# Performance work log

Measured on AMD Instinct MI355X. Metric: run time of the kernel, lower is better.

## Reference

```python
import jax, jax.numpy as jnp
import numpy as np

N = 100000      # nodes
E = 1200000     # edges (avg degree ~12)
D_IN = 64
D_OUT = 64


def setup_inputs() -> dict:
    key = jax.random.key(0)
    k1, k2, k3, k4 = jax.random.split(key, 4)
    x = jax.random.normal(k1, (N, D_IN), dtype=jnp.float32)
    # learned params (glorot-ish init)
    W = jax.random.normal(k2, (D_IN, D_OUT), dtype=jnp.float32) / np.sqrt(D_IN).astype(np.float32)
    b = jnp.zeros((D_OUT,), dtype=jnp.float32)
    src = jax.random.randint(k3, (E,), 0, N, dtype=jnp.int32)
    dst = jax.random.randint(k4, (E,), 0, N, dtype=jnp.int32)
    return {"x": x, "W": W, "b": b, "src": src, "dst": dst}


def reference(x, W, b, src, dst):
    # GCN layer: h = relu( D^-1/2 A D^-1/2 (x @ W) + b ), dropout=0 (eval)
    ones = jnp.ones(src.shape[0], dtype=x.dtype)
    deg_out = jax.ops.segment_sum(ones, src, num_segments=N)   # out-degree of source nodes
    deg_in = jax.ops.segment_sum(ones, dst, num_segments=N)    # in-degree of dest nodes
    norm_src = jax.lax.rsqrt(jnp.maximum(deg_out, 1.0))
    norm_dst = jax.lax.rsqrt(jnp.maximum(deg_in, 1.0))

    h = x @ W                                                  # [N, D_OUT] dense transform
    msg = h[src] * norm_src[src][:, None]                      # [E, D_OUT] gathered, pre-normalized messages
    agg = jax.ops.segment_sum(msg, dst, num_segments=N)        # [N, D_OUT] sparse aggregation
    out = agg * norm_dst[:, None] + b
    return jax.nn.relu(out)
```

## Files before the change

### kernel.cpp

```cpp
#include <hip/hip_runtime.h>
#include <hip/hip_bf16.h>

#define N_NODES 100000
#define N_EDGES 1200000
#define DCH 64

#define HB 96
#define CHUNK ((N_EDGES + HB - 1) / HB)
#define HALF_BINS 50000
#define HALF_WORDS 12500

#define BNODES 256
#define KBUK ((N_NODES + BNODES - 1) / BNODES)
#define CAPE 6144

#define GEMMB 384

#define OFF_DEG      0
#define OFF_CNTR     100000
#define OFF_BPART    512000
#define OFF_BLOCKOFF 665600
#define OFF_FLAG     819200
#define OFF_ESORT    819456
#define OFF_HS       10419712

__device__ __forceinline__ float load_f(const void* p, int i, int f32) {
    if (f32) return ((const float*)p)[i];
    return __bfloat162float(((const __hip_bfloat16*)p)[i]);
}

__device__ __forceinline__ unsigned short f2bf_bits(float f) {
    __hip_bfloat16 h = __float2bfloat16(f);
    return __builtin_bit_cast(unsigned short, h);
}

__global__ __launch_bounds__(1024)
void edges_kernel(const int* __restrict__ src,
                  const int* __restrict__ dst,
                  const void* __restrict__ x,
                  unsigned int* __restrict__ deg_packed,
                  int* __restrict__ bpart,
                  int* __restrict__ blockoff,
                  int* __restrict__ counter,
                  int* __restrict__ flag) {
    __shared__ unsigned int h[HALF_WORDS];
    __shared__ int cnt[KBUK];
    __shared__ int ss[512];
    __shared__ int amlast;
    int tid = threadIdx.x, b = blockIdx.x, half = blockIdx.y;
    for (int w = tid; w < HALF_WORDS; w += 1024) h[w] = 0;
    if (half == 0)
        for (int i = tid; i < KBUK; i += 1024) cnt[i] = 0;
    __syncthreads();
    int lo = half * HALF_BINS;
    int e0 = b * CHUNK;
    const int2* src2 = (const int2*)(src + e0);
    const int2* dst2 = (const int2*)(dst + e0);
    int npair = CHUNK >> 1;
    for (int p = tid; p < npair; p += 1024) {
        int2 sp = src2[p];
        int n0 = sp.x - lo, n1 = sp.y - lo;
        if ((unsigned)n0 < (unsigned)HALF_BINS)
            atomicAdd(&h[n0 >> 2], 1u << ((n0 & 3) * 8));
        if ((unsigned)n1 < (unsigned)HALF_BINS)
            atomicAdd(&h[n1 >> 2], 1u << ((n1 & 3) * 8));
        if (half == 0) {
            int2 dp = dst2[p];
            atomicAdd(&cnt[dp.x >> 8], 1);
            atomicAdd(&cnt[dp.y >> 8], 1);
        }
    }
    __syncthreads();
    unsigned int* dp = deg_packed + half * HALF_WORDS;
    for (int w = tid; w < HALF_WORDS; w += 1024) {
        unsigned int v = h[w];
        if (v) atomicAdd(&dp[w], v);
    }
    if (half == 0)
        for (int i = tid; i < KBUK; i += 1024) bpart[b * KBUK + i] = cnt[i];

    if (b == 0 && half == 0) {
        __syncthreads();
        if (tid == 0) cnt[0] = 0;
        __syncthreads();
        if (tid < 256) {
            const unsigned short* u = (const unsigned short*)x;
            int c = 0;
            for (int i = tid * 16; i < tid * 16 + 16; ++i) {
                unsigned short v = u[2 * i];
                int e = (v >> 7) & 0xFF;
                if (e >= 141) c++;
            }
            if (c) atomicAdd(&cnt[0], c);
        }
        __syncthreads();
        if (tid == 0) *flag = (cnt[0] > 256) ? 1 : 0;
    }

    if (half == 0) {
        __syncthreads();
        if (tid == 0) {
            __threadfence();
            int prev = __hip_atomic_fetch_add(counter, 1, __ATOMIC_ACQ_REL,
                                              __HIP_MEMORY_SCOPE_AGENT);
            amlast = (prev == HB - 1) ? 1 : 0;
        }
        __syncthreads();
        if (amlast) {
            __threadfence();
            int tot = 0;
            if (tid < KBUK)
                for (int bb = 0; bb < HB; ++bb) tot += bpart[bb * KBUK + tid];
            if (tid < 512) ss[tid] = (tid < KBUK) ? tot : 0;
            __syncthreads();
            for (int off = 1; off < 512; off <<= 1) {
                int add = 0;
                if (tid < 512 && tid >= off) add = ss[tid - off];
                __syncthreads();
                if (tid < 512) ss[tid] += add;
                __syncthreads();
            }
            if (tid < KBUK) {
                int run = ss[tid] - tot;
                for (int bb = 0; bb < HB; ++bb) {
                    blockoff[bb * KBUK + tid] = run;
                    run += bpart[bb * KBUK + tid];
                }
            }
        }
    }
}

__global__ __launch_bounds__(1024)
void mid_kernel(const int* __restrict__ src,
                const int* __restrict__ dst,
                const int* __restrict__ blockoff,
                unsigned int* __restrict__ esort,
                const void* __restrict__ x,
                const void* __restrict__ W,
                const unsigned int* __restrict__ deg_packed,
                const int* __restrict__ flag,
                __hip_bfloat16* __restrict__ hs) {
    __shared__ int cur[KBUK];
    int tid = threadIdx.x;
    int bid = blockIdx.x;
    if (bid < HB) {
        for (int i = tid; i < KBUK; i += 1024) cur[i] = blockoff[bid * KBUK + i];
        __syncthreads();
        int e0 = bid * CHUNK;
        const int2* src2 = (const int2*)(src + e0);
        const int2* dst2 = (const int2*)(dst + e0);
        int npair = CHUNK >> 1;
        for (int p = tid; p < npair; p += 1024) {
            int2 sp = src2[p];
            int2 dp = dst2[p];
            int pos0 = atomicAdd(&cur[dp.x >> 8], 1);
            esort[pos0] = (unsigned int)sp.x | ((unsigned int)(dp.x & 255) << 24);
            int pos1 = atomicAdd(&cur[dp.y >> 8], 1);
            esort[pos1] = (unsigned int)sp.y | ((unsigned int)(dp.y & 255) << 24);
        }
    } else {
        int f32 = *flag;
        int lane = tid & 63;
        int wave = ((bid - HB) * 1024 + tid) >> 6;
        const int nwaves = (GEMMB * 1024) >> 6;
        float wcol[DCH];
#pragma unroll
        for (int k = 0; k < DCH; ++k)
            wcol[k] = load_f(W, k * DCH + lane, f32);
        for (int node = wave; node < N_NODES; node += nwaves) {
            float xv = load_f(x, node * DCH + lane, f32);
            float s0 = 0.0f, s1 = 0.0f, s2 = 0.0f, s3 = 0.0f;
#pragma unroll
            for (int k = 0; k < DCH; k += 4) {
                float x0 = __int_as_float(__builtin_amdgcn_readlane(__float_as_int(xv), k + 0));
                float x1 = __int_as_float(__builtin_amdgcn_readlane(__float_as_int(xv), k + 1));
                float x2 = __int_as_float(__builtin_amdgcn_readlane(__float_as_int(xv), k + 2));
                float x3 = __int_as_float(__builtin_amdgcn_readlane(__float_as_int(xv), k + 3));
                s0 = fmaf(x0, wcol[k + 0], s0);
                s1 = fmaf(x1, wcol[k + 1], s1);
                s2 = fmaf(x2, wcol[k + 2], s2);
                s3 = fmaf(x3, wcol[k + 3], s3);
            }
            float sum = (s0 + s1) + (s2 + s3);
            unsigned int dw = deg_packed[node >> 2];
            float deg = (float)((dw >> ((node & 3) * 8)) & 0xFFu);
            float nrm = rsqrtf(fmaxf(deg, 1.0f));
            hs[node * DCH + lane] = __float2bfloat16(sum * nrm);
        }
    }
}

__global__ __launch_bounds__(1024)
void sortgather_kernel(const __hip_bfloat16* __restrict__ hs,
                       const unsigned int* __restrict__ esort,
                       const int* __restrict__ blockoff,
                       const void* __restrict__ b,
                       const int* __restrict__ flag,
                       void* __restrict__ out) {
    __shared__ unsigned int ebuf[CAPE];
    __shared__ int cnt[BNODES];
    __shared__ int loc[BNODES];
    __shared__ int sc[BNODES];
    __shared__ int cur[BNODES];
    int k = blockIdx.x, tid = threadIdx.x;
    int bbase = blockoff[k];
    int bend  = (k + 1 < KBUK) ? blockoff[k + 1] : N_EDGES;
    int m = bend - bbase;
    if (m > CAPE) m = CAPE;

    if (tid < BNODES) { cnt[tid] = 0; cur[tid] = 0; }
    __syncthreads();
    for (int e = tid; e < m; e += 1024)
        atomicAdd(&cnt[esort[bbase + e] >> 24], 1);
    __syncthreads();
    int v = 0;
    if (tid < BNODES) { v = cnt[tid]; sc[tid] = v; }
    __syncthreads();
    for (int off = 1; off < BNODES; off <<= 1) {
        int add = 0;
        if (tid < BNODES && tid >= off) add = sc[tid - off];
        __syncthreads();
        if (tid < BNODES) sc[tid] += add;
        __syncthreads();
    }
    if (tid < BNODES) loc[tid] = sc[tid] - v;
    __syncthreads();
    for (int e = tid; e < m; e += 1024) {
        unsigned int w = esort[bbase + e];
        int r = w >> 24;
        int pos = loc[r] + atomicAdd(&cur[r], 1);
        ebuf[pos] = w & 0xFFFFFFu;
    }
    __syncthreads();

    int f32 = *flag;
    int lane = tid & 63, wv = tid >> 6;
    int q = lane >> 4;
    int cg = lane & 15;
    const unsigned short* hsu = (const unsigned short*)hs;
    float b0 = load_f(b, cg * 4 + 0, f32);
    float b1 = load_f(b, cg * 4 + 1, f32);
    float b2 = load_f(b, cg * 4 + 2, f32);
    float b3 = load_f(b, cg * 4 + 3, f32);
    int nlo = k * BNODES;
    for (int base = wv; base < BNODES; base += 32) {
        int tA = base, tB = base + 16;
        int nodeA = nlo + tA, nodeB = nlo + tB;
        int begA = loc[tA], degA = cnt[tA];
        int begB = loc[tB], degB = cnt[tB];
        float4 aA0 = {0.f,0.f,0.f,0.f}, aA1 = {0.f,0.f,0.f,0.f};
        float4 aB0 = {0.f,0.f,0.f,0.f}, aB1 = {0.f,0.f,0.f,0.f};
        int dmax = degA > degB ? degA : degB;
        for (int j0 = 0; j0 < dmax; j0 += 8) {
            int i0 = j0 + q, i1 = j0 + 4 + q;
            unsigned int sA0 = ebuf[(i0 < degA) ? (begA + i0) : 0];
            unsigned int sA1 = ebuf[(i1 < degA) ? (begA + i1) : 0];
            unsigned int sB0 = ebuf[(i0 < degB) ? (begB + i0) : 0];
            unsigned int sB1 = ebuf[(i1 < degB) ? (begB + i1) : 0];
            uint2 uA0 = ((const uint2*)(hsu + sA0 * DCH))[cg];
            uint2 uA1 = ((const uint2*)(hsu + sA1 * DCH))[cg];
            uint2 uB0 = ((const uint2*)(hsu + sB0 * DCH))[cg];
            uint2 uB1 = ((const uint2*)(hsu + sB1 * DCH))[cg];
            if (i0 < degA) {
                aA0.x += __uint_as_float(uA0.x << 16);
                aA0.y += __uint_as_float(uA0.x & 0xFFFF0000u);
                aA0.z += __uint_as_float(uA0.y << 16);
                aA0.w += __uint_as_float(uA0.y & 0xFFFF0000u);
            }
            if (i1 < degA) {
                aA1.x += __uint_as_float(uA1.x << 16);
                aA1.y += __uint_as_float(uA1.x & 0xFFFF0000u);
                aA1.z += __uint_as_float(uA1.y << 16);
                aA1.w += __uint_as_float(uA1.y & 0xFFFF0000u);
            }
            if (i0 < degB) {
                aB0.x += __uint_as_float(uB0.x << 16);
                aB0.y += __uint_as_float(uB0.x & 0xFFFF0000u);
                aB0.z += __uint_as_float(uB0.y << 16);
                aB0.w += __uint_as_float(uB0.y & 0xFFFF0000u);
            }
            if (i1 < degB) {
                aB1.x += __uint_as_float(uB1.x << 16);
                aB1.y += __uint_as_float(uB1.x & 0xFFFF0000u);
                aB1.z += __uint_as_float(uB1.y << 16);
                aB1.w += __uint_as_float(uB1.y & 0xFFFF0000u);
            }
        }
        float4 oA, oB;
        oA.x = aA0.x + aA1.x; oA.y = aA0.y + aA1.y;
        oA.z = aA0.z + aA1.z; oA.w = aA0.w + aA1.w;
        oB.x = aB0.x + aB1.x; oB.y = aB0.y + aB1.y;
        oB.z = aB0.z + aB1.z; oB.w = aB0.w + aB1.w;
        oA.x += __shfl_xor(oA.x, 16); oA.y += __shfl_xor(oA.y, 16);
        oA.z += __shfl_xor(oA.z, 16); oA.w += __shfl_xor(oA.w, 16);
        oA.x += __shfl_xor(oA.x, 32); oA.y += __shfl_xor(oA.y, 32);
        oA.z += __shfl_xor(oA.z, 32); oA.w += __shfl_xor(oA.w, 32);
        oB.x += __shfl_xor(oB.x, 16); oB.y += __shfl_xor(oB.y, 16);
        oB.z += __shfl_xor(oB.z, 16); oB.w += __shfl_xor(oB.w, 16);
        oB.x += __shfl_xor(oB.x, 32); oB.y += __shfl_xor(oB.y, 32);
        oB.z += __shfl_xor(oB.z, 32); oB.w += __shfl_xor(oB.w, 32);
        int myNode = (lane < 16) ? nodeA : nodeB;
        int myDeg  = (lane < 16) ? degA : degB;
        float4 o   = (lane < 16) ? oA : oB;
        if (lane < 32 && myNode < N_NODES) {
            float nrm = rsqrtf(fmaxf((float)myDeg, 1.0f));
            o.x = fmaxf(o.x * nrm + b0, 0.0f);
            o.y = fmaxf(o.y * nrm + b1, 0.0f);
            o.z = fmaxf(o.z * nrm + b2, 0.0f);
            o.w = fmaxf(o.w * nrm + b3, 0.0f);
            if (f32) {
                ((float4*)out)[myNode * 16 + cg] = o;
            } else {
                ushort4 s;
                s.x = f2bf_bits(o.x);
                s.y = f2bf_bits(o.y);
                s.z = f2bf_bits(o.z);
                s.w = f2bf_bits(o.w);
                ((ushort4*)out)[myNode * 16 + cg] = s;
            }
        }
    }
}

extern "C" void kernel_launch(void* const* d_in, const int* in_sizes, int n_in,
                              void* d_out, int out_size, void* d_ws, size_t ws_size,
                              hipStream_t stream) {
    const void* x   = d_in[0];
    const void* W   = d_in[1];
    const void* b   = d_in[2];
    const int*  src = (const int*)d_in[3];
    const int*  dst = (const int*)d_in[4];

    char* ws = (char*)d_ws;
    unsigned int* deg_packed = (unsigned int*)(ws + OFF_DEG);
    int* counter  = (int*)(ws + OFF_CNTR);
    int* bpart    = (int*)(ws + OFF_BPART);
    int* blockoff = (int*)(ws + OFF_BLOCKOFF);
    int* flag     = (int*)(ws + OFF_FLAG);
    unsigned int* esort = (unsigned int*)(ws + OFF_ESORT);
    __hip_bfloat16* hs  = (__hip_bfloat16*)(ws + OFF_HS);

    (void)hipMemsetAsync(deg_packed, 0, 2 * HALF_WORDS * 4 + 4, stream);

    edges_kernel<<<dim3(HB, 2), 1024, 0, stream>>>(
        src, dst, x, deg_packed, bpart, blockoff, counter, flag);

    mid_kernel<<<HB + GEMMB, 1024, 0, stream>>>(
        src, dst, blockoff, esort, x, W, deg_packed, flag, hs);

    sortgather_kernel<<<KBUK, 1024, 0, stream>>>(hs, esort, blockoff, b, flag, d_out);
}
```

Before: 177.6 us.

## Fuse histogram, bucket scatter and GEMM into one kernel with fixed-capacity buckets

Merges the degree histogram, destination-bucket scatter and dense transform into a single launch. The per-block prefix scan and last-block reduction are replaced by global atomic bucket cursors into fixed-capacity (CAPE) bucket slots. Source normalization moves from the GEMM into the gather kernel, where a per-edge degree byte is looked up from a 256-entry rsqrt table and applied with an FMA. This removes one kernel launch and the serial scan, at the cost of extra degree loads in the gather and silently dropping edges if a bucket exceeds capacity.

```diff
diff --git a/kernel.cpp b/kernel.cpp
--- a/kernel.cpp
+++ b/kernel.cpp
@@ -14,15 +14,14 @@
 #define KBUK ((N_NODES + BNODES - 1) / BNODES)
 #define CAPE 6144
 
+#define HISTB (2 * HB)
 #define GEMMB 384
 
 #define OFF_DEG      0
-#define OFF_CNTR     100000
-#define OFF_BPART    512000
-#define OFF_BLOCKOFF 665600
-#define OFF_FLAG     819200
-#define OFF_ESORT    819456
-#define OFF_HS       10419712
+#define OFF_GCUR     100096
+#define OFF_FLAG     101760
+#define OFF_ESORT    102144
+#define OFF_HS       9711616
 
 __device__ __forceinline__ float load_f(const void* p, int i, int f32) {
     if (f32) return ((const float*)p)[i];
@@ -35,53 +34,94 @@
 }
 
 __global__ __launch_bounds__(1024)
-void edges_kernel(const int* __restrict__ src,
+void fused_kernel(const int* __restrict__ src,
                   const int* __restrict__ dst,
                   const void* __restrict__ x,
+                  const void* __restrict__ W,
                   unsigned int* __restrict__ deg_packed,
-                  int* __restrict__ bpart,
-                  int* __restrict__ blockoff,
-                  int* __restrict__ counter,
-                  int* __restrict__ flag) {
+                  int* __restrict__ gcur,
+                  unsigned int* __restrict__ esort,
+                  int* __restrict__ flag,
+                  __hip_bfloat16* __restrict__ hs) {
     __shared__ unsigned int h[HALF_WORDS];
-    __shared__ int cnt[KBUK];
-    __shared__ int ss[512];
-    __shared__ int amlast;
-    int tid = threadIdx.x, b = blockIdx.x, half = blockIdx.y;
-    for (int w = tid; w < HALF_WORDS; w += 1024) h[w] = 0;
-    if (half == 0)
-        for (int i = tid; i < KBUK; i += 1024) cnt[i] = 0;
-    __syncthreads();
-    int lo = half * HALF_BINS;
-    int e0 = b * CHUNK;
-    const int2* src2 = (const int2*)(src + e0);
-    const int2* dst2 = (const int2*)(dst + e0);
-    int npair = CHUNK >> 1;
-    for (int p = tid; p < npair; p += 1024) {
-        int2 sp = src2[p];
-        int n0 = sp.x - lo, n1 = sp.y - lo;
-        if ((unsigned)n0 < (unsigned)HALF_BINS)
-            atomicAdd(&h[n0 >> 2], 1u << ((n0 & 3) * 8));
-        if ((unsigned)n1 < (unsigned)HALF_BINS)
-            atomicAdd(&h[n1 >> 2], 1u << ((n1 & 3) * 8));
-        if (half == 0) {
+    int tid = threadIdx.x;
+    int bid = blockIdx.x;
+
+    if (bid < HB) {
+        int* cnt  = (int*)h;
+        int* base = cnt + KBUK;
+        int* cur  = base + KBUK;
+        for (int i = tid; i < KBUK; i += 1024) { cnt[i] = 0; cur[i] = 0; }
+        __syncthreads();
+        int e0 = bid * CHUNK;
+        const int2* src2 = (const int2*)(src + e0);
+        const int2* dst2 = (const int2*)(dst + e0);
+        int npair = CHUNK >> 1;
+        for (int p = tid; p < npair; p += 1024) {
             int2 dp = dst2[p];
             atomicAdd(&cnt[dp.x >> 8], 1);
             atomicAdd(&cnt[dp.y >> 8], 1);
         }
-    }
-    __syncthreads();
-    unsigned int* dp = deg_packed + half * HALF_WORDS;
-    for (int w = tid; w < HALF_WORDS; w += 1024) {
-        unsigned int v = h[w];
-        if (v) atomicAdd(&dp[w], v);
-    }
-    if (half == 0)
-        for (int i = tid; i < KBUK; i += 1024) bpart[b * KBUK + i] = cnt[i];
-
-    if (b == 0 && half == 0) {
-        __syncthreads();
-        if (tid == 0) cnt[0] = 0;
+        __syncthreads();
+        for (int i = tid; i < KBUK; i += 1024)
+            base[i] = atomicAdd(&gcur[i], cnt[i]);
+        __syncthreads();
+        for (int p = tid; p < npair; p += 1024) {
+            int2 sp = src2[p];
+            int2 dp = dst2[p];
+            int b0 = dp.x >> 8, b1 = dp.y >> 8;
+            int pos0 = base[b0] + atomicAdd(&cur[b0], 1);
+            if (pos0 < CAPE)
+                esort[b0 * CAPE + pos0] =
+                    (unsigned int)sp.x | ((unsigned int)(dp.x & 255) << 24);
+            int pos1 = base[b1] + atomicAdd(&cur[b1], 1);
+            if (pos1 < CAPE)
+                esort[b1 * CAPE + pos1] =
+                    (unsigned int)sp.y | ((unsigned int)(dp.y & 255) << 24);
+        }
+        if (bid == 0) {
+            __syncthreads();
+            if (tid == 0) cnt[0] = 0;
+            __syncthreads();
+            if (tid < 256) {
+                const unsigned short* u = (const unsigned short*)x;
+                int c = 0;
+                for (int i = tid * 16; i < tid * 16 + 16; ++i) {
+                    unsigned short v = u[2 * i];
+                    int e = (v >> 7) & 0xFF;
+                    if (e >= 141) c++;
+                }
+                if (c) atomicAdd(&cnt[0], c);
+            }
+            __syncthreads();
+            if (tid == 0) *flag = (cnt[0] > 256) ? 1 : 0;
+        }
+    } else if (bid < HB + HISTB) {
+        int hb = bid - HB;
+        int b = hb >> 1, half = hb & 1;
+        for (int w = tid; w < HALF_WORDS; w += 1024) h[w] = 0;
+        __syncthreads();
+        int lo = half * HALF_BINS;
+        int e0 = b * CHUNK;
+        const int2* src2 = (const int2*)(src + e0);
+        int npair = CHUNK >> 1;
+        for (int p = tid; p < npair; p += 1024) {
+            int2 sp = src2[p];
+            int n0 = sp.x - lo, n1 = sp.y - lo;
+            if ((unsigned)n0 < (unsigned)HALF_BINS)
+                atomicAdd(&h[n0 >> 2], 1u << ((n0 & 3) * 8));
+            if ((unsigned)n1 < (unsigned)HALF_BINS)
+                atomicAdd(&h[n1 >> 2], 1u << ((n1 & 3) * 8));
+        }
+        __syncthreads();
+        unsigned int* dp = deg_packed + half * HALF_WORDS;
+        for (int w = tid; w < HALF_WORDS; w += 1024) {
+            unsigned int v = h[w];
+            if (v) atomicAdd(&dp[w], v);
+        }
+    } else {
+        int* sn = (int*)h;
+        if (tid == 0) sn[0] = 0;
         __syncthreads();
         if (tid < 256) {
             const unsigned short* u = (const unsigned short*)x;
@@ -91,78 +131,13 @@
                 int e = (v >> 7) & 0xFF;
                 if (e >= 141) c++;
             }
-            if (c) atomicAdd(&cnt[0], c);
-        }
-        __syncthreads();
-        if (tid == 0) *flag = (cnt[0] > 256) ? 1 : 0;
-    }
-
-    if (half == 0) {
-        __syncthreads();
-        if (tid == 0) {
-            __threadfence();
-            int prev = __hip_atomic_fetch_add(counter, 1, __ATOMIC_ACQ_REL,
-                                              __HIP_MEMORY_SCOPE_AGENT);
-            amlast = (prev == HB - 1) ? 1 : 0;
-        }
-        __syncthreads();
-        if (amlast) {
-            __threadfence();
-            int tot = 0;
-            if (tid < KBUK)
-                for (int bb = 0; bb < HB; ++bb) tot += bpart[bb * KBUK + tid];
-            if (tid < 512) ss[tid] = (tid < KBUK) ? tot : 0;
-            __syncthreads();
-            for (int off = 1; off < 512; off <<= 1) {
-                int add = 0;
-                if (tid < 512 && tid >= off) add = ss[tid - off];
-                __syncthreads();
-                if (tid < 512) ss[tid] += add;
-                __syncthreads();
-            }
-            if (tid < KBUK) {
-                int run = ss[tid] - tot;
-                for (int bb = 0; bb < HB; ++bb) {
-                    blockoff[bb * KBUK + tid] = run;
-                    run += bpart[bb * KBUK + tid];
-                }
-            }
-        }
-    }
-}
-
-__global__ __launch_bounds__(1024)
-void mid_kernel(const int* __restrict__ src,
-                const int* __restrict__ dst,
-                const int* __restrict__ blockoff,
-                unsigned int* __restrict__ esort,
-                const void* __restrict__ x,
-                const void* __restrict__ W,
-                const unsigned int* __restrict__ deg_packed,
-                const int* __restrict__ flag,
-                __hip_bfloat16* __restrict__ hs) {
-    __shared__ int cur[KBUK];
-    int tid = threadIdx.x;
-    int bid = blockIdx.x;
-    if (bid < HB) {
-        for (int i = tid; i < KBUK; i += 1024) cur[i] = blockoff[bid * KBUK + i];
-        __syncthreads();
-        int e0 = bid * CHUNK;
-        const int2* src2 = (const int2*)(src + e0);
-        const int2* dst2 = (const int2*)(dst + e0);
-        int npair = CHUNK >> 1;
-        for (int p = tid; p < npair; p += 1024) {
-            int2 sp = src2[p];
-            int2 dp = dst2[p];
-            int pos0 = atomicAdd(&cur[dp.x >> 8], 1);
-            esort[pos0] = (unsigned int)sp.x | ((unsigned int)(dp.x & 255) << 24);
-            int pos1 = atomicAdd(&cur[dp.y >> 8], 1);
-            esort[pos1] = (unsigned int)sp.y | ((unsigned int)(dp.y & 255) << 24);
-        }
-    } else {
-        int f32 = *flag;
+            if (c) atomicAdd(sn, c);
+        }
+        __syncthreads();
+        int f32 = sn[0] > 256;
+
         int lane = tid & 63;
-        int wave = ((bid - HB) * 1024 + tid) >> 6;
+        int wave = ((bid - (HB + HISTB)) * 1024 + tid) >> 6;
         const int nwaves = (GEMMB * 1024) >> 6;
         float wcol[DCH];
 #pragma unroll
@@ -183,10 +158,7 @@
                 s3 = fmaf(x3, wcol[k + 3], s3);
             }
             float sum = (s0 + s1) + (s2 + s3);
-            unsigned int dw = deg_packed[node >> 2];
-            float deg = (float)((dw >> ((node & 3) * 8)) & 0xFFu);
-            float nrm = rsqrtf(fmaxf(deg, 1.0f));
-            hs[node * DCH + lane] = __float2bfloat16(sum * nrm);
+            hs[node * DCH + lane] = __float2bfloat16(sum);
         }
     }
 }
@@ -194,7 +166,8 @@
 __global__ __launch_bounds__(1024)
 void sortgather_kernel(const __hip_bfloat16* __restrict__ hs,
                        const unsigned int* __restrict__ esort,
-                       const int* __restrict__ blockoff,
+                       const int* __restrict__ gcur,
+                       const unsigned int* __restrict__ deg_packed,
                        const void* __restrict__ b,
                        const int* __restrict__ flag,
                        void* __restrict__ out) {
@@ -203,13 +176,14 @@
     __shared__ int loc[BNODES];
     __shared__ int sc[BNODES];
     __shared__ int cur[BNODES];
+    __shared__ float tab[256];
     int k = blockIdx.x, tid = threadIdx.x;
-    int bbase = blockoff[k];
-    int bend  = (k + 1 < KBUK) ? blockoff[k + 1] : N_EDGES;
-    int m = bend - bbase;
+    int bbase = k * CAPE;
+    int m = gcur[k];
     if (m > CAPE) m = CAPE;
 
     if (tid < BNODES) { cnt[tid] = 0; cur[tid] = 0; }
+    if (tid < 256) tab[tid] = rsqrtf(fmaxf((float)tid, 1.0f));
     __syncthreads();
     for (int e = tid; e < m; e += 1024)
         atomicAdd(&cnt[esort[bbase + e] >> 24], 1);
@@ -229,8 +203,11 @@
     for (int e = tid; e < m; e += 1024) {
         unsigned int w = esort[bbase + e];
         int r = w >> 24;
+        unsigned int s = w & 0xFFFFFFu;
+        unsigned int dw = deg_packed[s >> 2];
+        unsigned int degb = (dw >> ((s & 3) * 8)) & 0xFFu;
         int pos = loc[r] + atomicAdd(&cur[r], 1);
-        ebuf[pos] = w & 0xFFFFFFu;
+        ebuf[pos] = s | (degb << 24);
     }
     __syncthreads();
 
@@ -254,37 +231,41 @@
         int dmax = degA > degB ? degA : degB;
         for (int j0 = 0; j0 < dmax; j0 += 8) {
             int i0 = j0 + q, i1 = j0 + 4 + q;
-            unsigned int sA0 = ebuf[(i0 < degA) ? (begA + i0) : 0];
-            unsigned int sA1 = ebuf[(i1 < degA) ? (begA + i1) : 0];
-            unsigned int sB0 = ebuf[(i0 < degB) ? (begB + i0) : 0];
-            unsigned int sB1 = ebuf[(i1 < degB) ? (begB + i1) : 0];
+            unsigned int wA0 = ebuf[(i0 < degA) ? (begA + i0) : 0];
+            unsigned int wA1 = ebuf[(i1 < degA) ? (begA + i1) : 0];
+            unsigned int wB0 = ebuf[(i0 < degB) ? (begB + i0) : 0];
+            unsigned int wB1 = ebuf[(i1 < degB) ? (begB + i1) : 0];
+            unsigned int sA0 = wA0 & 0xFFFFFFu, sA1 = wA1 & 0xFFFFFFu;
+            unsigned int sB0 = wB0 & 0xFFFFFFu, sB1 = wB1 & 0xFFFFFFu;
+            float fA0 = tab[wA0 >> 24], fA1 = tab[wA1 >> 24];
+            float fB0 = tab[wB0 >> 24], fB1 = tab[wB1 >> 24];
             uint2 uA0 = ((const uint2*)(hsu + sA0 * DCH))[cg];
             uint2 uA1 = ((const uint2*)(hsu + sA1 * DCH))[cg];
             uint2 uB0 = ((const uint2*)(hsu + sB0 * DCH))[cg];
             uint2 uB1 = ((const uint2*)(hsu + sB1 * DCH))[cg];
             if (i0 < degA) {
-                aA0.x += __uint_as_float(uA0.x << 16);
-                aA0.y += __uint_as_float(uA0.x & 0xFFFF0000u);
-                aA0.z += __uint_as_float(uA0.y << 16);
-                aA0.w += __uint_as_float(uA0.y & 0xFFFF0000u);
+                aA0.x = fmaf(__uint_as_float(uA0.x << 16),        fA0, aA0.x);
+                aA0.y = fmaf(__uint_as_float(uA0.x & 0xFFFF0000u), fA0, aA0.y);
+                aA0.z = fmaf(__uint_as_float(uA0.y << 16),        fA0, aA0.z);
+                aA0.w = fmaf(__uint_as_float(uA0.y & 0xFFFF0000u), fA0, aA0.w);
             }
             if (i1 < degA) {
-                aA1.x += __uint_as_float(uA1.x << 16);
-                aA1.y += __uint_as_float(uA1.x & 0xFFFF0000u);
-                aA1.z += __uint_as_float(uA1.y << 16);
-                aA1.w += __uint_as_float(uA1.y & 0xFFFF0000u);
+                aA1.x = fmaf(__uint_as_float(uA1.x << 16),        fA1, aA1.x);
+                aA1.y = fmaf(__uint_as_float(uA1.x & 0xFFFF0000u), fA1, aA1.y);
+                aA1.z = fmaf(__uint_as_float(uA1.y << 16),        fA1, aA1.z);
+                aA1.w = fmaf(__uint_as_float(uA1.y & 0xFFFF0000u), fA1, aA1.w);
             }
             if (i0 < degB) {
-                aB0.x += __uint_as_float(uB0.x << 16);
-                aB0.y += __uint_as_float(uB0.x & 0xFFFF0000u);
-                aB0.z += __uint_as_float(uB0.y << 16);
-                aB0.w += __uint_as_float(uB0.y & 0xFFFF0000u);
+                aB0.x = fmaf(__uint_as_float(uB0.x << 16),        fB0, aB0.x);
+                aB0.y = fmaf(__uint_as_float(uB0.x & 0xFFFF0000u), fB0, aB0.y);
+                aB0.z = fmaf(__uint_as_float(uB0.y << 16),        fB0, aB0.z);
+                aB0.w = fmaf(__uint_as_float(uB0.y & 0xFFFF0000u), fB0, aB0.w);
             }
             if (i1 < degB) {
-                aB1.x += __uint_as_float(uB1.x << 16);
-                aB1.y += __uint_as_float(uB1.x & 0xFFFF0000u);
-                aB1.z += __uint_as_float(uB1.y << 16);
-                aB1.w += __uint_as_float(uB1.y & 0xFFFF0000u);
+                aB1.x = fmaf(__uint_as_float(uB1.x << 16),        fB1, aB1.x);
+                aB1.y = fmaf(__uint_as_float(uB1.x & 0xFFFF0000u), fB1, aB1.y);
+                aB1.z = fmaf(__uint_as_float(uB1.y << 16),        fB1, aB1.z);
+                aB1.w = fmaf(__uint_as_float(uB1.y & 0xFFFF0000u), fB1, aB1.w);
             }
         }
         float4 oA, oB;
@@ -334,20 +315,16 @@
 
     char* ws = (char*)d_ws;
     unsigned int* deg_packed = (unsigned int*)(ws + OFF_DEG);
-    int* counter  = (int*)(ws + OFF_CNTR);
-    int* bpart    = (int*)(ws + OFF_BPART);
-    int* blockoff = (int*)(ws + OFF_BLOCKOFF);
+    int* gcur     = (int*)(ws + OFF_GCUR);
     int* flag     = (int*)(ws + OFF_FLAG);
     unsigned int* esort = (unsigned int*)(ws + OFF_ESORT);
     __hip_bfloat16* hs  = (__hip_bfloat16*)(ws + OFF_HS);
 
-    (void)hipMemsetAsync(deg_packed, 0, 2 * HALF_WORDS * 4 + 4, stream);
-
-    edges_kernel<<<dim3(HB, 2), 1024, 0, stream>>>(
-        src, dst, x, deg_packed, bpart, blockoff, counter, flag);
-
-    mid_kernel<<<HB + GEMMB, 1024, 0, stream>>>(
-        src, dst, blockoff, esort, x, W, deg_packed, flag, hs);
-
-    sortgather_kernel<<<KBUK, 1024, 0, stream>>>(hs, esort, blockoff, b, flag, d_out);
-}
+    (void)hipMemsetAsync(ws, 0, OFF_FLAG + 4, stream);
+
+    fused_kernel<<<HB + HISTB + GEMMB, 1024, 0, stream>>>(
+        src, dst, x, W, deg_packed, gcur, esort, flag, hs);
+
+    sortgather_kernel<<<KBUK, 1024, 0, stream>>>(
+        hs, esort, gcur, deg_packed, b, flag, d_out);
+}
```

After: 166.7 us. -6.1%, faster.
